# Performance work log

Hardware: AMD Instinct MI355X
Metric: run time of the kernel (lower is better)

## Reference

```python
import jax, jax.numpy as jnp
import numpy as np

B, T, D = 2, 128, 1024
H, R, Dk, Dv = 8, 8, 64, 64


def setup_inputs() -> dict:
    key = jax.random.key(0)
    ks = jax.random.split(key, 11)
    w = lambda k, shp: jax.random.normal(k, shp, dtype=jnp.float32) * 0.02
    return {
        "hidden_states": jax.random.normal(ks[0], (B, T, D), dtype=jnp.float32),
        "Wq": w(ks[1], (D, H * Dk)),
        "Wk": w(ks[2], (D, H * Dk)),
        "Wv": w(ks[3], (D, H * Dv)),
        "Wb": w(ks[4], (D, H * R)),
        "Wtg": w(ks[5], (D, H * R)),
        "mode_logits": jax.random.normal(ks[6], (H, R), dtype=jnp.float32) * 0.1,
        "log_decay": jax.random.normal(ks[7], (H, R), dtype=jnp.float32) * 0.1,
        "omega_log_scale": jax.random.normal(ks[8], (H, R), dtype=jnp.float32) * 0.1,
        "Wg": w(ks[9], (D, H * Dv)),
        "Wo": w(ks[10], (H * Dv, D)),
    }


def _forward(x, Wq, Wk, Wv, Wb, Wtg, mode_logits, log_decay, omega_log_scale, Wg, Wo):
    b, t, _ = x.shape
    # projections
    q = (x @ Wq).reshape(b, t, H, Dk)
    k = (x @ Wk).reshape(b, t, H, Dk)
    v = (x @ Wv).reshape(b, t, H, Dv)
    beta = jax.nn.sigmoid((x @ Wb).reshape(b, t, H, R))
    tg = jax.nn.sigmoid((x @ Wtg).reshape(b, t, H, R))
    # spectral mode parameters
    pair_idx = jnp.arange(0, Dk, 2, dtype=jnp.float32)
    inv_freq = 1.0 / (10000.0 ** (pair_idx / Dk))            # [Dk/2]
    omega = jnp.exp(omega_log_scale)[..., None] * inv_freq    # [H,R,Dk/2]
    omega_full = jnp.repeat(omega, 2, axis=-1)                # [H,R,Dk] (repeat_interleave)
    cos_w = jnp.cos(omega_full)[None, :, :, None, :]          # [1,H,R,1,Dk]
    sin_w = jnp.sin(omega_full)[None, :, :, None, :]
    rho = jnp.exp(-jax.nn.softplus(log_decay))                # [H,R]
    mode_w = jax.nn.softmax(mode_logits, axis=-1)             # [H,R]

    # time-major for scan
    qT = jnp.moveaxis(q, 1, 0)
    kT = jnp.moveaxis(k, 1, 0)
    vT = jnp.moveaxis(v, 1, 0)
    betaT = jnp.moveaxis(beta, 1, 0)
    tgT = jnp.moveaxis(tg, 1, 0)

    def step(carry, xs):
        sr, si = carry                      # [B,H,R,Dv,Dk] each
        q_t, k_t, v_t, b_t, g_t = xs
        decay = (g_t * rho)[..., None, None]            # [B,H,R,1,1]
        rot_r = decay * (cos_w * sr - sin_w * si)
        rot_i = decay * (sin_w * sr + cos_w * si)
        pred = jnp.einsum('bhrvk,bhk->bhrv', rot_r, k_t)
        err = v_t[:, :, None, :] - pred                  # [B,H,R,Dv]
        write = err[..., None] * k_t[:, :, None, None, :]
        sr_new = rot_r + b_t[..., None, None] * write
        read = jnp.einsum('bhrvk,bhk->bhrv', sr_new, q_t)
        y = jnp.einsum('bhrv,hr->bhv', read, mode_w)     # [B,H,Dv]
        return (sr_new, rot_i), y

    s0 = jnp.zeros((b, H, R, Dv, Dk), dtype=x.dtype)
    _, ys = jax.lax.scan(step, (s0, s0), (qT, kT, vT, betaT, tgT))
    o = jnp.moveaxis(ys, 0, 1)                           # [B,T,H,Dv]
    gate = jax.nn.sigmoid((x @ Wg).reshape(b, t, H, Dv))
    o = (o * gate).reshape(b, t, H * Dv)
    return o @ Wo


def reference(hidden_states, Wq, Wk, Wv, Wb, Wtg, mode_logits, log_decay,
              omega_log_scale, Wg, Wo):
    return _forward(hidden_states, Wq, Wk, Wv, Wb, Wtg, mode_logits,
                    log_decay, omega_log_scale, Wg, Wo)
```

## Files before the change

### kernel.cpp

```cpp
#include <hip/hip_runtime.h>
#include <math.h>

#define T_ 128
#define NPROJ 2176
#define CH 32

typedef __attribute__((ext_vector_type(8))) short short8;
typedef __attribute__((ext_vector_type(4))) float float4v;

__device__ __forceinline__ ushort f2bf(float x) {
    unsigned u = __float_as_uint(x);
    u += 0x7FFF + ((u >> 16) & 1);
    return (ushort)(u >> 16);
}

__global__ __launch_bounds__(256) void prep_kernel(
    const float* __restrict__ x,
    const float* __restrict__ Wq, const float* __restrict__ Wk,
    const float* __restrict__ Wv, const float* __restrict__ Wb,
    const float* __restrict__ Wtg, const float* __restrict__ Wg,
    const float* __restrict__ Wo,
    const float* __restrict__ mode_logits, const float* __restrict__ log_decay,
    const float* __restrict__ ols,
    float* __restrict__ cosw, float* __restrict__ sinw,
    float* __restrict__ rho, float* __restrict__ modew,
    ushort* __restrict__ xb, ushort* __restrict__ wtb, ushort* __restrict__ wotb)
{
    __shared__ ushort tile[64][68];
    const int blk = blockIdx.x, tid = threadIdx.x;
    if (blk < 16) {
        int idx = blk * 256 + tid;
        if (idx >= 64 * 64) return;
        int t = idx >> 6;
        int k = idx & 63;
        int h = t >> 3;
        if (k == 0) {
            float ld = log_decay[t];
            rho[t] = 1.0f / (1.0f + expf(ld));
            float m = -1e30f;
            for (int i = 0; i < 8; i++) m = fmaxf(m, mode_logits[h * 8 + i]);
            float sum = 0.0f;
            for (int i = 0; i < 8; i++) sum += expf(mode_logits[h * 8 + i] - m);
            modew[t] = expf(mode_logits[t] - m) / sum;
        }
        float osc = expf(ols[t]);
        int p = k >> 1;
        float invf = expf(-((float)(2 * p) / 64.0f) * logf(10000.0f));
        float w = osc * invf;
        cosw[idx] = cosf(w);
        sinw[idx] = sinf(w);
        return;
    }
    if (blk < 80) {
        int base = (blk - 16) * 4096 + tid * 16;
        float4 f0 = *(const float4*)&x[base];
        float4 f1 = *(const float4*)&x[base + 4];
        float4 f2 = *(const float4*)&x[base + 8];
        float4 f3 = *(const float4*)&x[base + 12];
        short8 o0, o1;
        o0[0]=f2bf(f0.x); o0[1]=f2bf(f0.y); o0[2]=f2bf(f0.z); o0[3]=f2bf(f0.w);
        o0[4]=f2bf(f1.x); o0[5]=f2bf(f1.y); o0[6]=f2bf(f1.z); o0[7]=f2bf(f1.w);
        o1[0]=f2bf(f2.x); o1[1]=f2bf(f2.y); o1[2]=f2bf(f2.z); o1[3]=f2bf(f2.w);
        o1[4]=f2bf(f3.x); o1[5]=f2bf(f3.y); o1[6]=f2bf(f3.z); o1[7]=f2bf(f3.w);
        *(short8*)&xb[base] = o0;
        *(short8*)&xb[base + 8] = o1;
        return;
    }
    const float* src; int ld, c0, n0, k0, ldd; ushort* dst;
    if (blk < 624) {
        int b3 = blk - 80; int nt = b3 >> 4, kt = b3 & 15;
        n0 = nt * 64; k0 = kt * 64;
        if (n0 < 512)       { src = Wq;  c0 = n0;        ld = 512; }
        else if (n0 < 1024) { src = Wk;  c0 = n0 - 512;  ld = 512; }
        else if (n0 < 1536) { src = Wv;  c0 = n0 - 1024; ld = 512; }
        else if (n0 < 1600) { src = Wb;  c0 = n0 - 1536; ld = 64;  }
        else if (n0 < 1664) { src = Wtg; c0 = n0 - 1600; ld = 64;  }
        else                { src = Wg;  c0 = n0 - 1664; ld = 512; }
        dst = wtb; ldd = 1024;
    } else {
        int b4 = blk - 624; int nt = b4 >> 3, kt = b4 & 7;
        n0 = nt * 64; k0 = kt * 64;
        src = Wo; c0 = n0; ld = 1024; dst = wotb; ldd = 512;
    }
    #pragma unroll
    for (int rep = 0; rep < 4; rep++) {
        int k = rep * 16 + (tid >> 4);
        int nc = (tid & 15) * 4;
        float4 f = *(const float4*)&src[(size_t)(k0 + k) * ld + c0 + nc];
        tile[nc + 0][k] = f2bf(f.x);
        tile[nc + 1][k] = f2bf(f.y);
        tile[nc + 2][k] = f2bf(f.z);
        tile[nc + 3][k] = f2bf(f.w);
    }
    __syncthreads();
    #pragma unroll
    for (int rep = 0; rep < 4; rep++) {
        int n = rep * 16 + (tid >> 4);
        int kc = (tid & 15) * 4;
        uint2 u = *(const uint2*)&tile[n][kc];
        *(uint2*)&dst[(size_t)(n0 + n) * ldd + k0 + kc] = u;
    }
}

__global__ __launch_bounds__(256, 2) void proj_mfma(const ushort* __restrict__ Ab,
        const ushort* __restrict__ BTb, float* __restrict__ proj)
{
    __shared__ ushort sA[2][64][40];
    __shared__ ushort sB[2][64][40];
    const int n0 = blockIdx.x * 64, m0 = blockIdx.y * 64;
    const int tid = threadIdx.x;
    const int lane = tid & 63, w = tid >> 6;
    const int wm = w & 1, wn = w >> 1;
    const int l16 = lane & 15, quad = lane >> 4;
    const int srow = tid >> 2, skq = (tid & 3) * 8;
    const ushort* Ag = Ab + (size_t)(m0 + srow) * 1024 + skq;
    const ushort* Bg = BTb + (size_t)(n0 + srow) * 1024 + skq;
    short8 ra = *(const short8*)Ag;
    short8 rb = *(const short8*)Bg;
    float4v acc00 = {0,0,0,0}, acc01 = {0,0,0,0}, acc10 = {0,0,0,0}, acc11 = {0,0,0,0};
    for (int kt = 0; kt < 32; kt++) {
        const int cb = kt & 1;
        *(short8*)&sA[cb][srow][skq] = ra;
        *(short8*)&sB[cb][srow][skq] = rb;
        __syncthreads();
        if (kt + 1 < 32) {
            ra = *(const short8*)(Ag + (kt + 1) * 32);
            rb = *(const short8*)(Bg + (kt + 1) * 32);
        }
        short8 a0 = *(const short8*)&sA[cb][wm * 32 + l16][quad * 8];
        short8 a1 = *(const short8*)&sA[cb][wm * 32 + 16 + l16][quad * 8];
        short8 b0 = *(const short8*)&sB[cb][wn * 32 + l16][quad * 8];
        short8 b1 = *(const short8*)&sB[cb][wn * 32 + 16 + l16][quad * 8];
        acc00 = __builtin_amdgcn_mfma_f32_16x16x32_bf16(a0, b0, acc00, 0, 0, 0);
        acc01 = __builtin_amdgcn_mfma_f32_16x16x32_bf16(a0, b1, acc01, 0, 0, 0);
        acc10 = __builtin_amdgcn_mfma_f32_16x16x32_bf16(a1, b0, acc10, 0, 0, 0);
        acc11 = __builtin_amdgcn_mfma_f32_16x16x32_bf16(a1, b1, acc11, 0, 0, 0);
    }
    const bool sig = (n0 >= 1536);
    const int colb = n0 + wn * 32 + l16;
    const int rowb = m0 + wm * 32 + quad * 4;
    #pragma unroll
    for (int r2 = 0; r2 < 4; r2++) {
        float v00 = acc00[r2], v01 = acc01[r2], v10 = acc10[r2], v11 = acc11[r2];
        if (sig) {
            v00 = 1.0f / (1.0f + expf(-v00));
            v01 = 1.0f / (1.0f + expf(-v01));
            v10 = 1.0f / (1.0f + expf(-v10));
            v11 = 1.0f / (1.0f + expf(-v11));
        }
        proj[(size_t)(rowb + r2) * NPROJ + colb] = v00;
        proj[(size_t)(rowb + r2) * NPROJ + colb + 16] = v01;
        proj[(size_t)(rowb + 16 + r2) * NPROJ + colb] = v10;
        proj[(size_t)(rowb + 16 + r2) * NPROJ + colb + 16] = v11;
    }
}

__global__ __launch_bounds__(256, 2) void out_mfma(const ushort* __restrict__ Ab,
        const ushort* __restrict__ BTb, float* __restrict__ C)
{
    __shared__ ushort sA[2][64][40];
    __shared__ ushort sB[2][64][40];
    const int n0 = blockIdx.x * 64, m0 = blockIdx.y * 64;
    const int tid = threadIdx.x;
    const int lane = tid & 63, w = tid >> 6;
    const int wm = w & 1, wn = w >> 1;
    const int l16 = lane & 15, quad = lane >> 4;
    const int srow = tid >> 2, skq = (tid & 3) * 8;
    const ushort* Ag = Ab + (size_t)(m0 + srow) * 512 + skq;
    const ushort* Bg = BTb + (size_t)(n0 + srow) * 512 + skq;
    short8 ra = *(const short8*)Ag;
    short8 rb = *(const short8*)Bg;
    float4v acc00 = {0,0,0,0}, acc01 = {0,0,0,0}, acc10 = {0,0,0,0}, acc11 = {0,0,0,0};
    for (int kt = 0; kt < 16; kt++) {
        const int cb = kt & 1;
        *(short8*)&sA[cb][srow][skq] = ra;
        *(short8*)&sB[cb][srow][skq] = rb;
        __syncthreads();
        if (kt + 1 < 16) {
            ra = *(const short8*)(Ag + (kt + 1) * 32);
            rb = *(const short8*)(Bg + (kt + 1) * 32);
        }
        short8 a0 = *(const short8*)&sA[cb][wm * 32 + l16][quad * 8];
        short8 a1 = *(const short8*)&sA[cb][wm * 32 + 16 + l16][quad * 8];
        short8 b0 = *(const short8*)&sB[cb][wn * 32 + l16][quad * 8];
        short8 b1 = *(const short8*)&sB[cb][wn * 32 + 16 + l16][quad * 8];
        acc00 = __builtin_amdgcn_mfma_f32_16x16x32_bf16(a0, b0, acc00, 0, 0, 0);
        acc01 = __builtin_amdgcn_mfma_f32_16x16x32_bf16(a0, b1, acc01, 0, 0, 0);
        acc10 = __builtin_amdgcn_mfma_f32_16x16x32_bf16(a1, b0, acc10, 0, 0, 0);
        acc11 = __builtin_amdgcn_mfma_f32_16x16x32_bf16(a1, b1, acc11, 0, 0, 0);
    }
    const int colb = n0 + wn * 32 + l16;
    const int rowb = m0 + wm * 32 + quad * 4;
    #pragma unroll
    for (int r2 = 0; r2 < 4; r2++) {
        C[(size_t)(rowb + r2) * 1024 + colb] = acc00[r2];
        C[(size_t)(rowb + r2) * 1024 + colb + 16] = acc01[r2];
        C[(size_t)(rowb + 16 + r2) * 1024 + colb] = acc10[r2];
        C[(size_t)(rowb + 16 + r2) * 1024 + colb + 16] = acc11[r2];
    }
}

template<int CTRL>
__device__ __forceinline__ float dpp_add(float x) {
    int xi = __float_as_int(x);
    int yi = __builtin_amdgcn_update_dpp(xi, xi, CTRL, 0xF, 0xF, false);
    return x + __int_as_float(yi);
}

__global__ __launch_bounds__(256, 2) void scan_kernel(const float* __restrict__ proj,
        const float* __restrict__ cosw, const float* __restrict__ sinw,
        const float* __restrict__ rho, const float* __restrict__ modew,
        float* __restrict__ readbuf)
{
    __shared__ float qk[2][CH][128];
    __shared__ float vb[2][CH][16];
    __shared__ float bbuf[2][CH];
    __shared__ float gbuf[2][CH];

    const int bi = blockIdx.x;
    const int s  = bi & 3;
    const int hr = (bi >> 2) & 63;
    const int b  = bi >> 8;
    const int h = hr >> 3, r = hr & 7;
    const int tid = threadIdx.x;
    const int vl = tid >> 4;
    const int kl = tid & 15;

    float cw[4], sw[4];
    #pragma unroll
    for (int j = 0; j < 4; j++) {
        cw[j] = cosw[hr * 64 + kl * 4 + j];
        sw[j] = sinw[hr * 64 + kl * 4 + j];
    }
    const float rho_hr = rho[hr];
    const float mw = modew[hr];
    float sr[4] = {}, si[4] = {};

    const float* pb = proj + (size_t)b * T_ * NPROJ;
    const int qbase = h * 64;
    const int kbase = 512 + h * 64;
    const int vbase = 1024 + h * 64 + s * 16;
    const int boff  = 1536 + h * 8 + r;
    const int goff  = 1600 + h * 8 + r;

    auto stage = [&](int t0, int nb) {
        #pragma unroll
        for (int rep = 0; rep < 4; rep++) {
            int idx = rep * 256 + tid;
            int t = idx >> 5, sub = idx & 31;
            const float* row = pb + (size_t)(t0 + t) * NPROJ;
            float4 val = *(const float4*)(row + (sub < 16 ? qbase + sub * 4
                                                          : kbase + (sub - 16) * 4));
            *(float4*)&qk[nb][t][sub * 4] = val;
        }
        if (tid < 128) {
            int t = tid >> 2, sub = tid & 3;
            const float* row = pb + (size_t)(t0 + t) * NPROJ;
            *(float4*)&vb[nb][t][sub * 4] = *(const float4*)(row + vbase + sub * 4);
        } else if (tid < 160) {
            bbuf[nb][tid - 128] = pb[(size_t)(t0 + tid - 128) * NPROJ + boff];
        } else if (tid < 192) {
            gbuf[nb][tid - 160] = pb[(size_t)(t0 + tid - 160) * NPROJ + goff];
        }
    };

    stage(0, 0);
    __syncthreads();

    float* outp = readbuf + (size_t)(b * 64 + hr) * T_ * 64 + s * 16 + vl;

    for (int c = 0; c < T_ / CH; c++) {
        const int cb = c & 1;
        float kv[4], qv[4], vv, bt, gt;
        {
            float4 kf = *(const float4*)&qk[cb][0][64 + kl * 4];
            float4 qf = *(const float4*)&qk[cb][0][kl * 4];
            kv[0]=kf.x; kv[1]=kf.y; kv[2]=kf.z; kv[3]=kf.w;
            qv[0]=qf.x; qv[1]=qf.y; qv[2]=qf.z; qv[3]=qf.w;
            vv = vb[cb][0][vl]; bt = bbuf[cb][0]; gt = gbuf[cb][0];
        }
        if (c + 1 < T_ / CH) stage((c + 1) * CH, (c + 1) & 1);

        #pragma unroll 4
        for (int t = 0; t < CH; t++) {
            const int tn = (t + 1 < CH) ? t + 1 : t;
            float4 kf = *(const float4*)&qk[cb][tn][64 + kl * 4];
            float4 qf = *(const float4*)&qk[cb][tn][kl * 4];
            const float nvv = vb[cb][tn][vl];
            const float nbt = bbuf[cb][tn];
            const float ngt = gbuf[cb][tn];

            const float decay = gt * rho_hr;
            float rr[4];
            float pk = 0.0f, pq = 0.0f, kq = 0.0f;
            #pragma unroll
            for (int j = 0; j < 4; j++) {
                const float dc = decay * cw[j], ds = decay * sw[j];
                const float o_r = sr[j], o_i = si[j];
                rr[j] = dc * o_r - ds * o_i;
                si[j] = ds * o_r + dc * o_i;
                pk += rr[j] * kv[j];
                pq += rr[j] * qv[j];
                kq += kv[j] * qv[j];
            }
            pk = dpp_add<0xB1>(pk);  pq = dpp_add<0xB1>(pq);  kq = dpp_add<0xB1>(kq);
            pk = dpp_add<0x4E>(pk);  pq = dpp_add<0x4E>(pq);  kq = dpp_add<0x4E>(kq);
            pk = dpp_add<0x141>(pk); pq = dpp_add<0x141>(pq); kq = dpp_add<0x141>(kq);
            pk = dpp_add<0x140>(pk); pq = dpp_add<0x140>(pq); kq = dpp_add<0x140>(kq);

            const float sc = bt * (vv - pk);
            #pragma unroll
            for (int j = 0; j < 4; j++) sr[j] = rr[j] + sc * kv[j];
            const float rp = pq + sc * kq;
            if (kl == 0) outp[(size_t)(c * CH + t) * 64] = mw * rp;

            kv[0]=kf.x; kv[1]=kf.y; kv[2]=kf.z; kv[3]=kf.w;
            qv[0]=qf.x; qv[1]=qf.y; qv[2]=qf.z; qv[3]=qf.w;
            vv = nvv; bt = nbt; gt = ngt;
        }
        __syncthreads();
    }
}

__global__ void combine_kernel(const float* __restrict__ readbuf,
                               const float* __restrict__ proj,
                               ushort* __restrict__ Ab)
{
    int idx = blockIdx.x * 256 + threadIdx.x;
    if (idx >= 256 * 512) return;
    int bt = idx >> 9, c = idx & 511;
    int b = bt >> 7, t = bt & 127;
    int h = c >> 6, v = c & 63;
    float sacc = 0.0f;
    #pragma unroll
    for (int r = 0; r < 8; r++)
        sacc += readbuf[((size_t)(b * 64 + h * 8 + r) * 128 + t) * 64 + v];
    float gate = proj[(size_t)bt * NPROJ + 1664 + c];
    Ab[idx] = f2bf(gate * sacc);
}

extern "C" void kernel_launch(void* const* d_in, const int* in_sizes, int n_in,
                              void* d_out, int out_size, void* d_ws, size_t ws_size,
                              hipStream_t stream) {
    const float* x   = (const float*)d_in[0];
    const float* Wq  = (const float*)d_in[1];
    const float* Wk  = (const float*)d_in[2];
    const float* Wv  = (const float*)d_in[3];
    const float* Wb  = (const float*)d_in[4];
    const float* Wtg = (const float*)d_in[5];
    const float* ml  = (const float*)d_in[6];
    const float* ldc = (const float*)d_in[7];
    const float* ols = (const float*)d_in[8];
    const float* Wg  = (const float*)d_in[9];
    const float* Wo  = (const float*)d_in[10];
    float* out = (float*)d_out;

    float* ws = (float*)d_ws;
    float* proj    = ws;
    float* cosw    = proj + 256 * NPROJ;
    float* sinw    = cosw + 4096;
    float* rho     = sinw + 4096;
    float* modew   = rho + 64;
    ushort* xb     = (ushort*)(modew + 64);
    ushort* wotb   = (ushort*)((float*)xb + 131072);
    ushort* acombb = (ushort*)((float*)wotb + 262144);
    float* regionR = (float*)acombb + 65536;
    ushort* wtb    = (ushort*)regionR;
    float* readbuf = regionR;

    prep_kernel<<<752, 256, 0, stream>>>(x, Wq, Wk, Wv, Wb, Wtg, Wg, Wo,
                                         ml, ldc, ols, cosw, sinw, rho, modew,
                                         xb, wtb, wotb);
    proj_mfma<<<dim3(34, 4), 256, 0, stream>>>(xb, wtb, proj);
    scan_kernel<<<512, 256, 0, stream>>>(proj, cosw, sinw, rho, modew, readbuf);
    combine_kernel<<<512, 256, 0, stream>>>(readbuf, proj, acombb);
    out_mfma<<<dim3(16, 4), 256, 0, stream>>>(acombb, wotb, out);
}
```

Measured before the change: 146.7 us.

## Fuse combine into scan via gated atomic adds and precompute k·q per chunk

Drops the separate combine kernel. The scan now multiplies each mode's read by the output gate and atomically adds it into a zeroed fp32 buffer, which the prep kernel clears with extra blocks. The k·q dot product moves out of the per-step loop into a per-chunk precompute stored in shared memory, and the state update is written with packed float2 math. The output GEMM now converts the fp32 A operand to bf16 while loading it. The cost is 8-way atomic contention per output element, nondeterministic summation order, and an fp32 A buffer that doubles that GEMM's read traffic.

```diff
diff --git a/kernel.cpp b/kernel.cpp
--- a/kernel.cpp
+++ b/kernel.cpp
@@ -7,6 +7,7 @@
 
 typedef __attribute__((ext_vector_type(8))) short short8;
 typedef __attribute__((ext_vector_type(4))) float float4v;
+typedef __attribute__((ext_vector_type(2))) float float2v;
 
 __device__ __forceinline__ ushort f2bf(float x) {
     unsigned u = __float_as_uint(x);
@@ -24,7 +25,8 @@
     const float* __restrict__ ols,
     float* __restrict__ cosw, float* __restrict__ sinw,
     float* __restrict__ rho, float* __restrict__ modew,
-    ushort* __restrict__ xb, ushort* __restrict__ wtb, ushort* __restrict__ wotb)
+    ushort* __restrict__ xb, ushort* __restrict__ wtb, ushort* __restrict__ wotb,
+    float* __restrict__ Acomb)
 {
     __shared__ ushort tile[64][68];
     const int blk = blockIdx.x, tid = threadIdx.x;
@@ -64,6 +66,15 @@
         o1[4]=f2bf(f3.x); o1[5]=f2bf(f3.y); o1[6]=f2bf(f3.z); o1[7]=f2bf(f3.w);
         *(short8*)&xb[base] = o0;
         *(short8*)&xb[base + 8] = o1;
+        return;
+    }
+    if (blk >= 752) {
+        int base = (blk - 752) * 4096 + tid * 16;
+        float4 z = make_float4(0.f, 0.f, 0.f, 0.f);
+        *(float4*)&Acomb[base] = z;
+        *(float4*)&Acomb[base + 4] = z;
+        *(float4*)&Acomb[base + 8] = z;
+        *(float4*)&Acomb[base + 12] = z;
         return;
     }
     const float* src; int ld, c0, n0, k0, ldd; ushort* dst;
@@ -155,7 +166,138 @@
     }
 }
 
-__global__ __launch_bounds__(256, 2) void out_mfma(const ushort* __restrict__ Ab,
+template<int CTRL>
+__device__ __forceinline__ float dpp_add(float x) {
+    int xi = __float_as_int(x);
+    int yi = __builtin_amdgcn_update_dpp(xi, xi, CTRL, 0xF, 0xF, false);
+    return x + __int_as_float(yi);
+}
+
+__global__ __launch_bounds__(256, 2) void scan_kernel(const float* __restrict__ proj,
+        const float* __restrict__ cosw, const float* __restrict__ sinw,
+        const float* __restrict__ rho, const float* __restrict__ modew,
+        float* __restrict__ Acomb)
+{
+    __shared__ float qk[2][CH][128];
+    __shared__ float vbuf[2][CH][16];
+    __shared__ float gbuf[2][CH][16];
+    __shared__ float sc4[2][CH][4];
+
+    const int bi = blockIdx.x;
+    const int s  = bi & 3;
+    const int hr = (bi >> 2) & 63;
+    const int b  = bi >> 8;
+    const int h = hr >> 3, r = hr & 7;
+    const int tid = threadIdx.x;
+    const int vl = tid >> 4;
+    const int kl = tid & 15;
+
+    float2v cw0, cw1, sw0, sw1;
+    cw0.x = cosw[hr * 64 + kl * 4 + 0]; cw0.y = cosw[hr * 64 + kl * 4 + 1];
+    cw1.x = cosw[hr * 64 + kl * 4 + 2]; cw1.y = cosw[hr * 64 + kl * 4 + 3];
+    sw0.x = sinw[hr * 64 + kl * 4 + 0]; sw0.y = sinw[hr * 64 + kl * 4 + 1];
+    sw1.x = sinw[hr * 64 + kl * 4 + 2]; sw1.y = sinw[hr * 64 + kl * 4 + 3];
+    const float rho_hr = rho[hr];
+    const float mw = modew[hr];
+    float2v sr0 = {0,0}, sr1 = {0,0}, si0 = {0,0}, si1 = {0,0};
+
+    const float* pb = proj + (size_t)b * T_ * NPROJ;
+    const int qbase = h * 64;
+    const int kbase = 512 + h * 64;
+    const int vbase = 1024 + h * 64 + s * 16;
+    const int gbase = 1664 + h * 64 + s * 16;
+    const int boff  = 1536 + h * 8 + r;
+    const int goff  = 1600 + h * 8 + r;
+
+    auto stage = [&](int t0, int nb) {
+        #pragma unroll
+        for (int rep = 0; rep < 4; rep++) {
+            int idx = rep * 256 + tid;
+            int t = idx >> 5, sub = idx & 31;
+            const float* row = pb + (size_t)(t0 + t) * NPROJ;
+            float4 val = *(const float4*)(row + (sub < 16 ? qbase + sub * 4
+                                                          : kbase + (sub - 16) * 4));
+            *(float4*)&qk[nb][t][sub * 4] = val;
+        }
+        if (tid < 128) {
+            int t = tid >> 2, sub = tid & 3;
+            *(float4*)&vbuf[nb][t][sub * 4] =
+                *(const float4*)(pb + (size_t)(t0 + t) * NPROJ + vbase + sub * 4);
+        } else {
+            int t = (tid - 128) >> 2, sub = tid & 3;
+            *(float4*)&gbuf[nb][t][sub * 4] =
+                *(const float4*)(pb + (size_t)(t0 + t) * NPROJ + gbase + sub * 4);
+        }
+        if (tid < CH)            sc4[nb][tid][0]      = pb[(size_t)(t0 + tid) * NPROJ + boff];
+        else if (tid < 2 * CH)   sc4[nb][tid - CH][1] = pb[(size_t)(t0 + tid - CH) * NPROJ + goff];
+    };
+
+    stage(0, 0);
+    __syncthreads();
+
+    float* dst = Acomb + ((size_t)b * 128) * 512 + h * 64 + s * 16 + vl;
+
+    for (int c = 0; c < T_ / CH; c++) {
+        const int cb = c & 1;
+        {
+            int t = tid >> 3, j = tid & 7;
+            float4 ka = *(const float4*)&qk[cb][t][64 + j * 8];
+            float4 kb4 = *(const float4*)&qk[cb][t][64 + j * 8 + 4];
+            float4 qa = *(const float4*)&qk[cb][t][j * 8];
+            float4 qb4 = *(const float4*)&qk[cb][t][j * 8 + 4];
+            float p = ka.x * qa.x + ka.y * qa.y + ka.z * qa.z + ka.w * qa.w
+                    + kb4.x * qb4.x + kb4.y * qb4.y + kb4.z * qb4.z + kb4.w * qb4.w;
+            p = dpp_add<0xB1>(p);
+            p = dpp_add<0x4E>(p);
+            p = dpp_add<0x141>(p);
+            if (j == 0) sc4[cb][t][2] = p;
+        }
+        __syncthreads();
+        if (c + 1 < T_ / CH) stage((c + 1) * CH, (c + 1) & 1);
+
+        #pragma unroll 4
+        for (int t = 0; t < CH; t++) {
+            float4 kf = *(const float4*)&qk[cb][t][64 + kl * 4];
+            float4 qf = *(const float4*)&qk[cb][t][kl * 4];
+            float4 sv = *(const float4*)&sc4[cb][t][0];
+            const float vv = vbuf[cb][t][vl];
+            const float gate = gbuf[cb][t][vl];
+
+            const float decay = sv.y * rho_hr;
+            float2v k0; k0.x = kf.x; k0.y = kf.y;
+            float2v k1; k1.x = kf.z; k1.y = kf.w;
+            float2v q0; q0.x = qf.x; q0.y = qf.y;
+            float2v q1; q1.x = qf.z; q1.y = qf.w;
+
+            float2v t1 = cw0 * sr0 - sw0 * si0;
+            float2v u1 = sw0 * sr0 + cw0 * si0;
+            float2v t2 = cw1 * sr1 - sw1 * si1;
+            float2v u2 = sw1 * sr1 + cw1 * si1;
+            float2v d2; d2.x = decay; d2.y = decay;
+            float2v rr0 = d2 * t1, rr1 = d2 * t2;
+            si0 = d2 * u1; si1 = d2 * u2;
+
+            float2v pk2 = rr0 * k0 + rr1 * k1;
+            float2v pq2 = rr0 * q0 + rr1 * q1;
+            float pk = pk2.x + pk2.y;
+            float pq = pq2.x + pq2.y;
+            pk = dpp_add<0xB1>(pk);  pq = dpp_add<0xB1>(pq);
+            pk = dpp_add<0x4E>(pk);  pq = dpp_add<0x4E>(pq);
+            pk = dpp_add<0x141>(pk); pq = dpp_add<0x141>(pq);
+            pk = dpp_add<0x140>(pk); pq = dpp_add<0x140>(pq);
+
+            const float sc = sv.x * (vv - pk);
+            float2v sc2; sc2.x = sc; sc2.y = sc;
+            sr0 = rr0 + sc2 * k0;
+            sr1 = rr1 + sc2 * k1;
+            const float rp = pq + sc * sv.z;
+            if (kl == 0) atomicAdd(dst + (size_t)(c * CH + t) * 512, mw * rp * gate);
+        }
+        __syncthreads();
+    }
+}
+
+__global__ __launch_bounds__(256, 2) void out_mfma(const float* __restrict__ Af,
         const ushort* __restrict__ BTb, float* __restrict__ C)
 {
     __shared__ ushort sA[2][64][40];
@@ -166,18 +308,23 @@
     const int wm = w & 1, wn = w >> 1;
     const int l16 = lane & 15, quad = lane >> 4;
     const int srow = tid >> 2, skq = (tid & 3) * 8;
-    const ushort* Ag = Ab + (size_t)(m0 + srow) * 512 + skq;
+    const float* Ag = Af + (size_t)(m0 + srow) * 512 + skq;
     const ushort* Bg = BTb + (size_t)(n0 + srow) * 512 + skq;
-    short8 ra = *(const short8*)Ag;
+    float4 fa0 = *(const float4*)Ag;
+    float4 fa1 = *(const float4*)(Ag + 4);
     short8 rb = *(const short8*)Bg;
     float4v acc00 = {0,0,0,0}, acc01 = {0,0,0,0}, acc10 = {0,0,0,0}, acc11 = {0,0,0,0};
     for (int kt = 0; kt < 16; kt++) {
         const int cb = kt & 1;
+        short8 ra;
+        ra[0]=f2bf(fa0.x); ra[1]=f2bf(fa0.y); ra[2]=f2bf(fa0.z); ra[3]=f2bf(fa0.w);
+        ra[4]=f2bf(fa1.x); ra[5]=f2bf(fa1.y); ra[6]=f2bf(fa1.z); ra[7]=f2bf(fa1.w);
         *(short8*)&sA[cb][srow][skq] = ra;
         *(short8*)&sB[cb][srow][skq] = rb;
         __syncthreads();
         if (kt + 1 < 16) {
-            ra = *(const short8*)(Ag + (kt + 1) * 32);
+            fa0 = *(const float4*)(Ag + (kt + 1) * 32);
+            fa1 = *(const float4*)(Ag + (kt + 1) * 32 + 4);
             rb = *(const short8*)(Bg + (kt + 1) * 32);
         }
         short8 a0 = *(const short8*)&sA[cb][wm * 32 + l16][quad * 8];
@@ -198,145 +345,6 @@
         C[(size_t)(rowb + 16 + r2) * 1024 + colb] = acc10[r2];
         C[(size_t)(rowb + 16 + r2) * 1024 + colb + 16] = acc11[r2];
     }
-}
-
-template<int CTRL>
-__device__ __forceinline__ float dpp_add(float x) {
-    int xi = __float_as_int(x);
-    int yi = __builtin_amdgcn_update_dpp(xi, xi, CTRL, 0xF, 0xF, false);
-    return x + __int_as_float(yi);
-}
-
-__global__ __launch_bounds__(256, 2) void scan_kernel(const float* __restrict__ proj,
-        const float* __restrict__ cosw, const float* __restrict__ sinw,
-        const float* __restrict__ rho, const float* __restrict__ modew,
-        float* __restrict__ readbuf)
-{
-    __shared__ float qk[2][CH][128];
-    __shared__ float vb[2][CH][16];
-    __shared__ float bbuf[2][CH];
-    __shared__ float gbuf[2][CH];
-
-    const int bi = blockIdx.x;
-    const int s  = bi & 3;
-    const int hr = (bi >> 2) & 63;
-    const int b  = bi >> 8;
-    const int h = hr >> 3, r = hr & 7;
-    const int tid = threadIdx.x;
-    const int vl = tid >> 4;
-    const int kl = tid & 15;
-
-    float cw[4], sw[4];
-    #pragma unroll
-    for (int j = 0; j < 4; j++) {
-        cw[j] = cosw[hr * 64 + kl * 4 + j];
-        sw[j] = sinw[hr * 64 + kl * 4 + j];
-    }
-    const float rho_hr = rho[hr];
-    const float mw = modew[hr];
-    float sr[4] = {}, si[4] = {};
-
-    const float* pb = proj + (size_t)b * T_ * NPROJ;
-    const int qbase = h * 64;
-    const int kbase = 512 + h * 64;
-    const int vbase = 1024 + h * 64 + s * 16;
-    const int boff  = 1536 + h * 8 + r;
-    const int goff  = 1600 + h * 8 + r;
-
-    auto stage = [&](int t0, int nb) {
-        #pragma unroll
-        for (int rep = 0; rep < 4; rep++) {
-            int idx = rep * 256 + tid;
-            int t = idx >> 5, sub = idx & 31;
-            const float* row = pb + (size_t)(t0 + t) * NPROJ;
-            float4 val = *(const float4*)(row + (sub < 16 ? qbase + sub * 4
-                                                          : kbase + (sub - 16) * 4));
-            *(float4*)&qk[nb][t][sub * 4] = val;
-        }
-        if (tid < 128) {
-            int t = tid >> 2, sub = tid & 3;
-            const float* row = pb + (size_t)(t0 + t) * NPROJ;
-            *(float4*)&vb[nb][t][sub * 4] = *(const float4*)(row + vbase + sub * 4);
-        } else if (tid < 160) {
-            bbuf[nb][tid - 128] = pb[(size_t)(t0 + tid - 128) * NPROJ + boff];
-        } else if (tid < 192) {
-            gbuf[nb][tid - 160] = pb[(size_t)(t0 + tid - 160) * NPROJ + goff];
-        }
-    };
-
-    stage(0, 0);
-    __syncthreads();
-
-    float* outp = readbuf + (size_t)(b * 64 + hr) * T_ * 64 + s * 16 + vl;
-
-    for (int c = 0; c < T_ / CH; c++) {
-        const int cb = c & 1;
-        float kv[4], qv[4], vv, bt, gt;
-        {
-            float4 kf = *(const float4*)&qk[cb][0][64 + kl * 4];
-            float4 qf = *(const float4*)&qk[cb][0][kl * 4];
-            kv[0]=kf.x; kv[1]=kf.y; kv[2]=kf.z; kv[3]=kf.w;
-            qv[0]=qf.x; qv[1]=qf.y; qv[2]=qf.z; qv[3]=qf.w;
-            vv = vb[cb][0][vl]; bt = bbuf[cb][0]; gt = gbuf[cb][0];
-        }
-        if (c + 1 < T_ / CH) stage((c + 1) * CH, (c + 1) & 1);
-
-        #pragma unroll 4
-        for (int t = 0; t < CH; t++) {
-            const int tn = (t + 1 < CH) ? t + 1 : t;
-            float4 kf = *(const float4*)&qk[cb][tn][64 + kl * 4];
-            float4 qf = *(const float4*)&qk[cb][tn][kl * 4];
-            const float nvv = vb[cb][tn][vl];
-            const float nbt = bbuf[cb][tn];
-            const float ngt = gbuf[cb][tn];
-
-            const float decay = gt * rho_hr;
-            float rr[4];
-            float pk = 0.0f, pq = 0.0f, kq = 0.0f;
-            #pragma unroll
-            for (int j = 0; j < 4; j++) {
-                const float dc = decay * cw[j], ds = decay * sw[j];
-                const float o_r = sr[j], o_i = si[j];
-                rr[j] = dc * o_r - ds * o_i;
-                si[j] = ds * o_r + dc * o_i;
-                pk += rr[j] * kv[j];
-                pq += rr[j] * qv[j];
-                kq += kv[j] * qv[j];
-            }
-            pk = dpp_add<0xB1>(pk);  pq = dpp_add<0xB1>(pq);  kq = dpp_add<0xB1>(kq);
-            pk = dpp_add<0x4E>(pk);  pq = dpp_add<0x4E>(pq);  kq = dpp_add<0x4E>(kq);
-            pk = dpp_add<0x141>(pk); pq = dpp_add<0x141>(pq); kq = dpp_add<0x141>(kq);
-            pk = dpp_add<0x140>(pk); pq = dpp_add<0x140>(pq); kq = dpp_add<0x140>(kq);
-
-            const float sc = bt * (vv - pk);
-            #pragma unroll
-            for (int j = 0; j < 4; j++) sr[j] = rr[j] + sc * kv[j];
-            const float rp = pq + sc * kq;
-            if (kl == 0) outp[(size_t)(c * CH + t) * 64] = mw * rp;
-
-            kv[0]=kf.x; kv[1]=kf.y; kv[2]=kf.z; kv[3]=kf.w;
-            qv[0]=qf.x; qv[1]=qf.y; qv[2]=qf.z; qv[3]=qf.w;
-            vv = nvv; bt = nbt; gt = ngt;
-        }
-        __syncthreads();
-    }
-}
-
-__global__ void combine_kernel(const float* __restrict__ readbuf,
-                               const float* __restrict__ proj,
-                               ushort* __restrict__ Ab)
-{
-    int idx = blockIdx.x * 256 + threadIdx.x;
-    if (idx >= 256 * 512) return;
-    int bt = idx >> 9, c = idx & 511;
-    int b = bt >> 7, t = bt & 127;
-    int h = c >> 6, v = c & 63;
-    float sacc = 0.0f;
-    #pragma unroll
-    for (int r = 0; r < 8; r++)
-        sacc += readbuf[((size_t)(b * 64 + h * 8 + r) * 128 + t) * 64 + v];
-    float gate = proj[(size_t)bt * NPROJ + 1664 + c];
-    Ab[idx] = f2bf(gate * sacc);
 }
 
 extern "C" void kernel_launch(void* const* d_in, const int* in_sizes, int n_in,
@@ -363,16 +371,13 @@
     float* modew   = rho + 64;
     ushort* xb     = (ushort*)(modew + 64);
     ushort* wotb   = (ushort*)((float*)xb + 131072);
-    ushort* acombb = (ushort*)((float*)wotb + 262144);
-    float* regionR = (float*)acombb + 65536;
-    ushort* wtb    = (ushort*)regionR;
-    float* readbuf = regionR;
-
-    prep_kernel<<<752, 256, 0, stream>>>(x, Wq, Wk, Wv, Wb, Wtg, Wg, Wo,
+    float*  Acomb  = (float*)wotb + 262144;
+    ushort* wtb    = (ushort*)(Acomb + 131072);
+
+    prep_kernel<<<784, 256, 0, stream>>>(x, Wq, Wk, Wv, Wb, Wtg, Wg, Wo,
                                          ml, ldc, ols, cosw, sinw, rho, modew,
-                                         xb, wtb, wotb);
+                                         xb, wtb, wotb, Acomb);
     proj_mfma<<<dim3(34, 4), 256, 0, stream>>>(xb, wtb, proj);
-    scan_kernel<<<512, 256, 0, stream>>>(proj, cosw, sinw, rho, modew, readbuf);
-    combine_kernel<<<512, 256, 0, stream>>>(readbuf, proj, acombb);
-    out_mfma<<<dim3(16, 4), 256, 0, stream>>>(acombb, wotb, out);
-}
+    scan_kernel<<<512, 256, 0, stream>>>(proj, cosw, sinw, rho, modew, Acomb);
+    out_mfma<<<dim3(16, 4), 256, 0, stream>>>(Acomb, wotb, out);
+}
```

New measurement: 140.2 us. 4.4% less time.
